# Kernel optimization log

Hardware: AMD Instinct MI355X
Metric: run time of the kernel (lower is better)

## Reference

```python
import jax, jax.numpy as jnp
import numpy as np

DIM = 1024
NUM_HEADS = 16
HEAD_DIM = DIM // NUM_HEADS


def setup_inputs() -> dict:
    key = jax.random.key(0)
    k1, k2, k3, k4, k5, k6 = jax.random.split(key, 6)
    B, T, C = 4, 2048, DIM
    s = 1.0 / np.sqrt(C)
    return {
        "x": jax.random.normal(k1, (B, T, C), dtype=jnp.float32),
        "attn_bias": jax.random.normal(k2, (B, T, T), dtype=jnp.float32),
        "qkv_w": jax.random.uniform(k3, (3 * C, C), dtype=jnp.float32, minval=-s, maxval=s),
        "qkv_b": jax.random.uniform(k4, (3 * C,), dtype=jnp.float32, minval=-s, maxval=s),
        "out_w": jax.random.uniform(k5, (C, C), dtype=jnp.float32, minval=-s, maxval=s),
        "out_b": jax.random.uniform(k6, (C,), dtype=jnp.float32, minval=-s, maxval=s),
    }


def reference(x, attn_bias, qkv_w, qkv_b, out_w, out_b):
    B, T, C = x.shape
    H, D = NUM_HEADS, HEAD_DIM
    # fused QKV projection (torch Linear: x @ W^T + b)
    qkv = jnp.einsum('btc,fc->btf', x, qkv_w) + qkv_b  # [B,T,3C]
    q, k, v = jnp.split(qkv, 3, axis=-1)
    q = q.reshape(B, T, H, D).transpose(0, 2, 1, 3)  # [B,H,T,D]
    k = k.reshape(B, T, H, D).transpose(0, 2, 1, 3)
    v = v.reshape(B, T, H, D).transpose(0, 2, 1, 3)
    scores = jnp.einsum('bhtd,bhsd->bhts', q, k) / jnp.sqrt(jnp.float32(D))
    scores = scores + attn_bias[:, None, :, :]  # 3-D bias -> broadcast over heads
    attn = jax.nn.softmax(scores, axis=-1)
    out = jnp.einsum('bhts,bhsd->bhtd', attn, v)  # [B,H,T,D]
    out = out.transpose(0, 2, 1, 3).reshape(B, T, C)
    return jnp.einsum('btc,fc->btf', out, out_w) + out_b
```

## Files before the change

kernel.cpp:

```cpp
#include <hip/hip_runtime.h>

#define BATCH 4
#define SEQ   2048
#define CDIM  1024
#define HEADS 16
#define HDIM  64
#define N3    3072
#define NTOK  8192
#define QKP   2048
#define LOG2E 1.44269504f
#define QSC   0.18033688f

typedef __attribute__((ext_vector_type(4))) float    float4v;
typedef __attribute__((ext_vector_type(8))) short    short8;
typedef __attribute__((ext_vector_type(8))) __bf16   bf16x8;
typedef __attribute__((ext_vector_type(4))) _Float16 half4v;
typedef __attribute__((ext_vector_type(2))) _Float16 half2v;

__device__ __forceinline__ unsigned short f2bf(float f) {
    union { float f; unsigned int u; } x; x.f = f;
    unsigned int r = x.u + 0x7fffu + ((x.u >> 16) & 1u);
    return (unsigned short)(r >> 16);
}

__device__ __forceinline__ bf16x8 ld_bf8(const unsigned short* p) {
    short8 s = *(const short8*)p;
    return __builtin_bit_cast(bf16x8, s);
}

__device__ __forceinline__ void glds16(const void* g, void* l) {
    __builtin_amdgcn_global_load_lds(
        (const __attribute__((address_space(1))) void*)g,
        (__attribute__((address_space(3))) void*)l, 16, 0, 0);
}

__global__ void cast_f32_bf16(const float* __restrict__ in,
                              unsigned short* __restrict__ out, int n4) {
    int i = blockIdx.x * blockDim.x + threadIdx.x;
    if (i >= n4) return;
    float4v v = ((const float4v*)in)[i];
    ushort4 r;
    r.x = f2bf(v[0]); r.y = f2bf(v[1]); r.z = f2bf(v[2]); r.w = f2bf(v[3]);
    ((ushort4*)out)[i] = r;
}

__global__ __launch_bounds__(256, 3)
void gemm_bt(const unsigned short* __restrict__ A,
             const unsigned short* __restrict__ Bm,
             const float* __restrict__ bias,
             void* __restrict__ Cout,
             void* __restrict__ Cout2,
             int M, int N, int K, int mode)
{
    __shared__ alignas(16) unsigned short SMEM[2 * 128 * 64];
    unsigned short* As = SMEM;
    unsigned short* Bs = SMEM + 128 * 64;

    const int tid  = threadIdx.x;
    const int lane = tid & 63;
    const int wave = tid >> 6;
    const int wr = wave >> 1, wc = wave & 1;
    const int lm = lane & 15, quad = lane >> 4;

    const int nwg  = gridDim.x * gridDim.y;
    const int d    = blockIdx.y * gridDim.x + blockIdx.x;
    const int orig = (d & 7) * (nwg >> 3) + (d >> 3);
    const int bix  = orig % gridDim.x;
    const int biy  = orig / gridDim.x;

    const size_t m0 = (size_t)biy * 128;
    const size_t n0 = (size_t)bix * 128;

    const unsigned short* ag[4];
    const unsigned short* bg[4];
    unsigned short* la[4];
    unsigned short* lb[4];
#pragma unroll
    for (int i = 0; i < 4; i++) {
        int idx = tid + i * 256;
        int row = idx >> 3;
        int lc  = (idx & 7) ^ (row & 7);
        ag[i] = &A [(m0 + row) * K + lc * 8];
        bg[i] = &Bm[(n0 + row) * K + lc * 8];
        la[i] = &As[(idx & ~63) * 8];
        lb[i] = &Bs[(idx & ~63) * 8];
    }

    float4v acc[4][4];
#pragma unroll
    for (int i = 0; i < 4; i++)
#pragma unroll
        for (int j = 0; j < 4; j++) acc[i][j] = (float4v){0.f, 0.f, 0.f, 0.f};

    for (int k0 = 0; k0 < K; k0 += 64) {
#pragma unroll
        for (int i = 0; i < 4; i++) glds16(ag[i], la[i]);
#pragma unroll
        for (int i = 0; i < 4; i++) glds16(bg[i], lb[i]);
#pragma unroll
        for (int i = 0; i < 4; i++) { ag[i] += 64; bg[i] += 64; }
        __syncthreads();
#pragma unroll
        for (int kk = 0; kk < 2; kk++) {
            bf16x8 af[4], bfr[4];
#pragma unroll
            for (int t = 0; t < 4; t++) {
                int slot = ((quad + kk * 4) ^ (lm & 7)) * 8;
                af [t] = ld_bf8(&As[(wr * 64 + t * 16 + lm) * 64 + slot]);
                bfr[t] = ld_bf8(&Bs[(wc * 64 + t * 16 + lm) * 64 + slot]);
            }
#pragma unroll
            for (int ti = 0; ti < 4; ti++)
#pragma unroll
                for (int tj = 0; tj < 4; tj++)
                    acc[ti][tj] = __builtin_amdgcn_mfma_f32_16x16x32_bf16(
                        af[ti], bfr[tj], acc[ti][tj], 0, 0, 0);
        }
        __syncthreads();
    }

    const bool vpath = (mode == 1) && ((int)n0 >= 2 * CDIM);

    if (!vpath) {
#pragma unroll
        for (int ti = 0; ti < 4; ti++) {
            size_t row = m0 + wr * 64 + ti * 16 + quad * 4;
#pragma unroll
            for (int tj = 0; tj < 4; tj++) {
                int col = (int)n0 + wc * 64 + tj * 16 + lm;
                float bv = bias[col];
                if (mode == 0) {
#pragma unroll
                    for (int r = 0; r < 4; r++)
                        ((float*)Cout)[(row + r) * N + col] = acc[ti][tj][r] + bv;
                } else {
                    float scl = (col < CDIM) ? QSC : 1.0f;
#pragma unroll
                    for (int r = 0; r < 4; r++)
                        ((unsigned short*)Cout)[(row + r) * QKP + col] =
                            f2bf((acc[ti][tj][r] + bv) * scl);
                }
            }
        }
    } else {
        half4v hv[4][4];
#pragma unroll
        for (int ti = 0; ti < 4; ti++)
#pragma unroll
            for (int tj = 0; tj < 4; tj++) {
                int col = (int)n0 + wc * 64 + tj * 16 + lm;
                float bv = bias[col];
#pragma unroll
                for (int r = 0; r < 4; r++)
                    hv[ti][tj][r] = (_Float16)(acc[ti][tj][r] + bv);
            }

        const int bbv = (int)(m0 >> 11);
        const int s0  = (int)(m0 & 2047);
        unsigned short* LT = SMEM;

#pragma unroll
        for (int p = 0; p < 2; ++p) {
            __syncthreads();
            if (wc == p) {
#pragma unroll
                for (int ti = 0; ti < 4; ti++) {
                    int ssb = wr * 64 + ti * 16 + quad * 4;
                    int p16 = (ssb >> 3);
                    int w8  = (ssb >> 2) & 1;
#pragma unroll
                    for (int tj = 0; tj < 4; tj++) {
                        int dd = tj * 16 + lm;
                        *(half4v*)&LT[dd * 136 + ((p16 ^ (dd & 15)) * 8) + w8 * 4] =
                            hv[ti][tj];
                    }
                }
            }
            __syncthreads();
#pragma unroll
            for (int i = 0; i < 4; ++i) {
                int dd   = i * 16 + (tid >> 4);
                int ss16 = tid & 15;
                short8 val = *(const short8*)&LT[dd * 136 + ((ss16 ^ (dd & 15)) * 8)];
                size_t gr = (size_t)bbv * CDIM + ((int)n0 - 2 * CDIM) + p * 64 + dd;
                *(short8*)((unsigned short*)Cout2 + gr * SEQ + s0 + ss16 * 8) = val;
            }
        }
    }
}

__global__ __launch_bounds__(256, 4)
void attn_kernel(const unsigned short* __restrict__ qk,
                 const unsigned short* __restrict__ vT,
                 const float* __restrict__ bias,
                 unsigned short* __restrict__ outp)
{
    __shared__ alignas(16) char smem[32768];
    float*          BiasS = (float*)smem;
    unsigned short* Qs    = (unsigned short*)smem;
    unsigned short* Ks    = (unsigned short*)(smem + 16384);
    unsigned short* Vts   = (unsigned short*)(smem + 24576);

    const int tid  = threadIdx.x;
    const int lane = tid & 63, wave = tid >> 6;
    const int lm = lane & 15, quad = lane >> 4;
    const int q0 = blockIdx.x * 64;
    const int bh = blockIdx.y;
    const int bb = bh >> 4, h = bh & 15;
    const size_t rowbase = (size_t)bb * SEQ;
    const unsigned short* vTh = vT + (size_t)bh * HDIM * SEQ;
    const float* biasb = bias + (size_t)bb * SEQ * SEQ + (size_t)q0 * SEQ;

#pragma unroll
    for (int i = 0; i < 2; i++) {
        int idx = tid + i * 256;
        int row = idx >> 3;
        int lc  = (idx & 7) ^ (row & 7);
        glds16(&qk[(rowbase + q0 + row) * QKP + h * 64 + lc * 8], &Qs[(idx & ~63) * 8]);
    }
    __syncthreads();
    bf16x8 bq[2];
#pragma unroll
    for (int kk = 0; kk < 2; kk++)
        bq[kk] = ld_bf8(&Qs[(wave * 16 + lm) * 64 + (((quad + kk * 4) ^ (lm & 7)) * 8)]);

    const unsigned short *kg0, *kg1, *vg0, *vg1;
    unsigned short *lk0, *lk1, *lv0, *lv1;
    {
        int idx = tid, row = idx >> 3, lc = (idx & 7) ^ (row & 7);
        kg0 = &qk[(rowbase + row) * QKP + CDIM + h * 64 + lc * 8];
        vg0 = &vTh[(size_t)row * SEQ + lc * 8];
        lk0 = &Ks[(idx & ~63) * 8];
        lv0 = &Vts[(idx & ~63) * 8];
        idx = tid + 256; row = idx >> 3; lc = (idx & 7) ^ (row & 7);
        kg1 = &qk[(rowbase + row) * QKP + CDIM + h * 64 + lc * 8];
        vg1 = &vTh[(size_t)row * SEQ + lc * 8];
        lk1 = &Ks[(idx & ~63) * 8];
        lv1 = &Vts[(idx & ~63) * 8];
    }
    const float* bgp[4];
    float*       lbp[4];
#pragma unroll
    for (int i = 0; i < 4; i++) {
        int idx = tid + i * 256;
        int row = idx >> 4;
        int lc  = (idx & 15) ^ (row & 15);
        bgp[i] = &biasb[(size_t)row * SEQ + lc * 4];
        lbp[i] = &BiasS[(idx & ~63) * 4];
    }

    const half4v vones = {(_Float16)1.f, (_Float16)1.f, (_Float16)1.f, (_Float16)1.f};
    float4v rs4 = (float4v){0.f, 0.f, 0.f, 0.f};
    float4v o[4];
#pragma unroll
    for (int t = 0; t < 4; t++) o[t] = (float4v){0.f, 0.f, 0.f, 0.f};

    for (int it = 0; it < SEQ / 64; ++it) {
        __syncthreads();
        glds16(kg0, lk0); glds16(kg1, lk1);
        glds16(vg0, lv0); glds16(vg1, lv1);
#pragma unroll
        for (int i = 0; i < 4; i++) glds16(bgp[i], lbp[i]);
        kg0 += 64 * QKP; kg1 += 64 * QKP;
        vg0 += 64; vg1 += 64;
#pragma unroll
        for (int i = 0; i < 4; i++) bgp[i] += 64;
        __syncthreads();

        float4v st[4];
#pragma unroll
        for (int tj = 0; tj < 4; ++tj) {
            float4v bv = *(const float4v*)&BiasS[(wave * 16 + lm) * 64 +
                                                 (((tj * 4 + quad) ^ lm) * 4)];
            st[tj] = bv * LOG2E;
            bf16x8 ak0 = ld_bf8(&Ks[(tj * 16 + lm) * 64 + (((quad    ) ^ (lm & 7)) * 8)]);
            bf16x8 ak1 = ld_bf8(&Ks[(tj * 16 + lm) * 64 + (((quad + 4) ^ (lm & 7)) * 8)]);
            st[tj] = __builtin_amdgcn_mfma_f32_16x16x32_bf16(ak0, bq[0], st[tj], 0, 0, 0);
            st[tj] = __builtin_amdgcn_mfma_f32_16x16x32_bf16(ak1, bq[1], st[tj], 0, 0, 0);
        }

        half4v pa[4];
#pragma unroll
        for (int tj = 0; tj < 4; ++tj) {
            float p0 = __builtin_amdgcn_exp2f(st[tj][0]);
            float p1 = __builtin_amdgcn_exp2f(st[tj][1]);
            float p2 = __builtin_amdgcn_exp2f(st[tj][2]);
            float p3 = __builtin_amdgcn_exp2f(st[tj][3]);
            half2v plo = __builtin_bit_cast(half2v, __builtin_amdgcn_cvt_pkrtz(p0, p1));
            half2v phi = __builtin_bit_cast(half2v, __builtin_amdgcn_cvt_pkrtz(p2, p3));
            pa[tj][0] = plo[0]; pa[tj][1] = plo[1];
            pa[tj][2] = phi[0]; pa[tj][3] = phi[1];
        }

#pragma unroll
        for (int tj = 0; tj < 4; ++tj)
            rs4 = __builtin_amdgcn_mfma_f32_16x16x16f16(pa[tj], vones, rs4, 0, 0, 0);

        __builtin_amdgcn_s_setprio(1);
#pragma unroll
        for (int tj = 0; tj < 4; ++tj) {
            int c = tj * 4 + quad;
#pragma unroll
            for (int dt = 0; dt < 4; ++dt) {
                int row = dt * 16 + lm;
                int off = (((c >> 1) ^ (lm & 7)) * 8) + (c & 1) * 4;
                half4v vb = *(const half4v*)&Vts[row * 64 + off];
                o[dt] = __builtin_amdgcn_mfma_f32_16x16x16f16(pa[tj], vb, o[dt], 0, 0, 0);
            }
        }
        __builtin_amdgcn_s_setprio(0);
    }

    float i4[4];
#pragma unroll
    for (int r = 0; r < 4; r++) i4[r] = 1.0f / rs4[r];
#pragma unroll
    for (int dt = 0; dt < 4; dt++) {
        int col = h * 64 + dt * 16 + lm;
#pragma unroll
        for (int r = 0; r < 4; r++) {
            size_t trow = rowbase + q0 + wave * 16 + quad * 4 + r;
            outp[trow * CDIM + col] = f2bf(o[dt][r] * i4[r]);
        }
    }
}

extern "C" void kernel_launch(void* const* d_in, const int* in_sizes, int n_in,
                              void* d_out, int out_size, void* d_ws, size_t ws_size,
                              hipStream_t stream)
{
    const float* x         = (const float*)d_in[0];
    const float* attn_bias = (const float*)d_in[1];
    const float* qkv_w     = (const float*)d_in[2];
    const float* qkv_b     = (const float*)d_in[3];
    const float* out_w     = (const float*)d_in[4];
    const float* out_b     = (const float*)d_in[5];
    float* out = (float*)d_out;

    char* p = (char*)d_ws;
    unsigned short* x_bf   = (unsigned short*)p; p += (size_t)NTOK * CDIM * 2;
    unsigned short* wq_bf  = (unsigned short*)p; p += (size_t)N3 * CDIM * 2;
    unsigned short* wo_bf  = (unsigned short*)p; p += (size_t)CDIM * CDIM * 2;
    unsigned short* qk_bf  = (unsigned short*)p; p += (size_t)NTOK * QKP * 2;
    unsigned short* vT_f16 = (unsigned short*)p; p += (size_t)BATCH * CDIM * SEQ * 2;
    unsigned short* at_bf  = (unsigned short*)p;

    int n4;
    n4 = NTOK * CDIM / 4;
    cast_f32_bf16<<<(n4 + 255) / 256, 256, 0, stream>>>(x, x_bf, n4);
    n4 = N3 * CDIM / 4;
    cast_f32_bf16<<<(n4 + 255) / 256, 256, 0, stream>>>(qkv_w, wq_bf, n4);
    n4 = CDIM * CDIM / 4;
    cast_f32_bf16<<<(n4 + 255) / 256, 256, 0, stream>>>(out_w, wo_bf, n4);

    gemm_bt<<<dim3(N3 / 128, NTOK / 128), 256, 0, stream>>>(
        x_bf, wq_bf, qkv_b, qk_bf, vT_f16, NTOK, N3, CDIM, 1);

    attn_kernel<<<dim3(SEQ / 64, BATCH * HEADS), 256, 0, stream>>>(
        qk_bf, vT_f16, attn_bias, at_bf);

    gemm_bt<<<dim3(CDIM / 128, NTOK / 128), 256, 0, stream>>>(
        at_bf, wo_bf, out_b, out, nullptr, NTOK, CDIM, CDIM, 0);
}
```

Baseline: 352.7 us.

## Use 16x16x32 f16 MFMA for PV with permuted V^T layout; merge cast kernels

The attention P·V product and the row-sum now use the K=32 f16 MFMA instead of the K=16 variant, halving the MFMA instruction count and using 8-wide LDS loads of V. To match the new operand register layout, the QKV GEMM epilogue writes V^T with a permuted column order, pairing 4-element chunks 16 columns apart. The three fp32-to-bf16 cast launches are also merged into one kernel to cut launch overhead. The risk is that the permutation must exactly match the MFMA k-index mapping, or results become wrong.

```diff
diff --git a/kernel.cpp b/kernel.cpp
--- a/kernel.cpp
+++ b/kernel.cpp
@@ -15,6 +15,7 @@
 typedef __attribute__((ext_vector_type(8))) short    short8;
 typedef __attribute__((ext_vector_type(8))) __bf16   bf16x8;
 typedef __attribute__((ext_vector_type(4))) _Float16 half4v;
+typedef __attribute__((ext_vector_type(8))) _Float16 half8v;
 typedef __attribute__((ext_vector_type(2))) _Float16 half2v;
 
 __device__ __forceinline__ unsigned short f2bf(float f) {
@@ -34,14 +35,22 @@
         (__attribute__((address_space(3))) void*)l, 16, 0, 0);
 }
 
-__global__ void cast_f32_bf16(const float* __restrict__ in,
-                              unsigned short* __restrict__ out, int n4) {
+__global__ void cast3_f32_bf16(const float* __restrict__ a, int na4,
+                               const float* __restrict__ b, int nb4,
+                               const float* __restrict__ c, int nc4,
+                               unsigned short* __restrict__ oa,
+                               unsigned short* __restrict__ ob,
+                               unsigned short* __restrict__ oc) {
     int i = blockIdx.x * blockDim.x + threadIdx.x;
-    if (i >= n4) return;
-    float4v v = ((const float4v*)in)[i];
+    const float* src; unsigned short* dst; int j = i;
+    if (j < na4)            { src = a; dst = oa; }
+    else if ((j -= na4) < nb4) { src = b; dst = ob; }
+    else if ((j -= nb4) < nc4) { src = c; dst = oc; }
+    else return;
+    float4v v = ((const float4v*)src)[j];
     ushort4 r;
     r.x = f2bf(v[0]); r.y = f2bf(v[1]); r.z = f2bf(v[2]); r.w = f2bf(v[3]);
-    ((ushort4*)out)[i] = r;
+    ((ushort4*)dst)[j] = r;
 }
 
 __global__ __launch_bounds__(256, 3)
@@ -180,10 +189,20 @@
 #pragma unroll
             for (int i = 0; i < 4; ++i) {
                 int dd   = i * 16 + (tid >> 4);
-                int ss16 = tid & 15;
-                short8 val = *(const short8*)&LT[dd * 136 + ((ss16 ^ (dd & 15)) * 8)];
+                int u16  = tid & 15;
+                int win  = u16 >> 3, u = u16 & 7;
+                int base = (u < 4) ? u : (u + 4);
+                int ssa  = win * 64 + base * 4;
+                int ssb2 = ssa + 16;
+                half4v va = *(const half4v*)&LT[dd * 136 +
+                    (((ssa >> 3) ^ (dd & 15)) * 8) + ((ssa >> 2) & 1) * 4];
+                half4v vb = *(const half4v*)&LT[dd * 136 +
+                    (((ssb2 >> 3) ^ (dd & 15)) * 8) + ((ssb2 >> 2) & 1) * 4];
+                half8v vv;
+                vv[0] = va[0]; vv[1] = va[1]; vv[2] = va[2]; vv[3] = va[3];
+                vv[4] = vb[0]; vv[5] = vb[1]; vv[6] = vb[2]; vv[7] = vb[3];
                 size_t gr = (size_t)bbv * CDIM + ((int)n0 - 2 * CDIM) + p * 64 + dd;
-                *(short8*)((unsigned short*)Cout2 + gr * SEQ + s0 + ss16 * 8) = val;
+                *(half8v*)((unsigned short*)Cout2 + gr * SEQ + s0 + u16 * 8) = vv;
             }
         }
     }
@@ -249,7 +268,8 @@
         lbp[i] = &BiasS[(idx & ~63) * 4];
     }
 
-    const half4v vones = {(_Float16)1.f, (_Float16)1.f, (_Float16)1.f, (_Float16)1.f};
+    const half8v vones8 = {(_Float16)1.f, (_Float16)1.f, (_Float16)1.f, (_Float16)1.f,
+                           (_Float16)1.f, (_Float16)1.f, (_Float16)1.f, (_Float16)1.f};
     float4v rs4 = (float4v){0.f, 0.f, 0.f, 0.f};
     float4v o[4];
 #pragma unroll
@@ -279,7 +299,7 @@
             st[tj] = __builtin_amdgcn_mfma_f32_16x16x32_bf16(ak1, bq[1], st[tj], 0, 0, 0);
         }
 
-        half4v pa[4];
+        half8v pq[2];
 #pragma unroll
         for (int tj = 0; tj < 4; ++tj) {
             float p0 = __builtin_amdgcn_exp2f(st[tj][0]);
@@ -288,24 +308,24 @@
             float p3 = __builtin_amdgcn_exp2f(st[tj][3]);
             half2v plo = __builtin_bit_cast(half2v, __builtin_amdgcn_cvt_pkrtz(p0, p1));
             half2v phi = __builtin_bit_cast(half2v, __builtin_amdgcn_cvt_pkrtz(p2, p3));
-            pa[tj][0] = plo[0]; pa[tj][1] = plo[1];
-            pa[tj][2] = phi[0]; pa[tj][3] = phi[1];
-        }
-
-#pragma unroll
-        for (int tj = 0; tj < 4; ++tj)
-            rs4 = __builtin_amdgcn_mfma_f32_16x16x16f16(pa[tj], vones, rs4, 0, 0, 0);
+            pq[tj >> 1][(tj & 1) * 4 + 0] = plo[0];
+            pq[tj >> 1][(tj & 1) * 4 + 1] = plo[1];
+            pq[tj >> 1][(tj & 1) * 4 + 2] = phi[0];
+            pq[tj >> 1][(tj & 1) * 4 + 3] = phi[1];
+        }
+
+        rs4 = __builtin_amdgcn_mfma_f32_16x16x32_f16(pq[0], vones8, rs4, 0, 0, 0);
+        rs4 = __builtin_amdgcn_mfma_f32_16x16x32_f16(pq[1], vones8, rs4, 0, 0, 0);
 
         __builtin_amdgcn_s_setprio(1);
 #pragma unroll
-        for (int tj = 0; tj < 4; ++tj) {
-            int c = tj * 4 + quad;
+        for (int tjp = 0; tjp < 2; ++tjp) {
 #pragma unroll
             for (int dt = 0; dt < 4; ++dt) {
                 int row = dt * 16 + lm;
-                int off = (((c >> 1) ^ (lm & 7)) * 8) + (c & 1) * 4;
-                half4v vb = *(const half4v*)&Vts[row * 64 + off];
-                o[dt] = __builtin_amdgcn_mfma_f32_16x16x16f16(pa[tj], vb, o[dt], 0, 0, 0);
+                half8v v8 = *(const half8v*)&Vts[row * 64 +
+                               (((tjp * 4 + quad) ^ (lm & 7)) * 8)];
+                o[dt] = __builtin_amdgcn_mfma_f32_16x16x32_f16(pq[tjp], v8, o[dt], 0, 0, 0);
             }
         }
         __builtin_amdgcn_s_setprio(0);
@@ -345,13 +365,12 @@
     unsigned short* vT_f16 = (unsigned short*)p; p += (size_t)BATCH * CDIM * SEQ * 2;
     unsigned short* at_bf  = (unsigned short*)p;
 
-    int n4;
-    n4 = NTOK * CDIM / 4;
-    cast_f32_bf16<<<(n4 + 255) / 256, 256, 0, stream>>>(x, x_bf, n4);
-    n4 = N3 * CDIM / 4;
-    cast_f32_bf16<<<(n4 + 255) / 256, 256, 0, stream>>>(qkv_w, wq_bf, n4);
-    n4 = CDIM * CDIM / 4;
-    cast_f32_bf16<<<(n4 + 255) / 256, 256, 0, stream>>>(out_w, wo_bf, n4);
+    const int na4 = NTOK * CDIM / 4;
+    const int nb4 = N3 * CDIM / 4;
+    const int nc4 = CDIM * CDIM / 4;
+    const int nt4 = na4 + nb4 + nc4;
+    cast3_f32_bf16<<<(nt4 + 255) / 256, 256, 0, stream>>>(
+        x, na4, qkv_w, nb4, out_w, nc4, x_bf, wq_bf, wo_bf);
 
     gemm_bt<<<dim3(N3 / 128, NTOK / 128), 256, 0, stream>>>(
         x_bf, wq_bf, qkv_b, qk_bf, vT_f16, NTOK, N3, CDIM, 1);
```

After: 348.6 us. About the same (-1.2%).
